# Kernel optimization log

Hardware: AMD Instinct MI355X
Metric: run time of the kernel (lower is better)

The kernel has to match this reference:

```python
import jax, jax.numpy as jnp
import numpy as np

EMBED_DIM = 1024
ATTN_DIM = 128
B, S = 4, 2048


def setup_inputs() -> dict:
    key = jax.random.key(0)
    k1, k2, k3, k4 = jax.random.split(key, 4)
    embedded = jax.random.normal(k1, (B, S, EMBED_DIM), dtype=jnp.float32)
    # torch nn.Linear weights are [out_features, in_features]
    scale = 1.0 / np.sqrt(EMBED_DIM)
    Wk = jax.random.uniform(k2, (ATTN_DIM, EMBED_DIM), dtype=jnp.float32, minval=-scale, maxval=scale)
    Wq = jax.random.uniform(k3, (ATTN_DIM, EMBED_DIM), dtype=jnp.float32, minval=-scale, maxval=scale)
    Wv = jax.random.uniform(k4, (ATTN_DIM, EMBED_DIM), dtype=jnp.float32, minval=-scale, maxval=scale)
    return {"embedded": embedded, "Wk": Wk, "Wq": Wq, "Wv": Wv}


def reference(embedded, Wk, Wq, Wv):
    # projections (no bias): x @ W.T
    k = jnp.einsum('bse,ae->bsa', embedded, Wk)  # [B,S,A]
    q = jnp.einsum('bse,ae->bsa', embedded, Wq)
    v = jnp.einsum('bse,ae->bsa', embedded, Wv)
    ad = k.shape[-1]
    scores = jnp.einsum('bqa,bka->bqk', q, k) / jnp.sqrt(jnp.float32(ad))  # [B,S,S]
    causal = jnp.tril(jnp.ones((scores.shape[1], scores.shape[1]), dtype=bool))
    scores = jnp.where(causal, scores, -jnp.inf)
    probs = jax.nn.softmax(scores, axis=-1)
    out = jnp.einsum('bqk,bka->bqa', probs, v)
    return jnp.round(out, 4)
```

## Files before the change

kernel.cpp:

```cpp
#include <hip/hip_runtime.h>
#include <hip/hip_bf16.h>
#include <math.h>

#define B 4
#define S 2048
#define E 1024
#define A 128
#define CHUNK 256
#define NCHMAX 8

typedef __attribute__((ext_vector_type(8))) short short8;
typedef __attribute__((ext_vector_type(4))) float floatx4;

static __device__ __forceinline__ short f2bf(float f) {
  union { float f; unsigned u; } c;
  c.f = f;
  unsigned r = (c.u + 0x7fffu + ((c.u >> 16) & 1u)) >> 16;
  return (short)r;
}
static __device__ __forceinline__ unsigned f2bf2(float x, float y) {
  __hip_bfloat162 h = __float22bfloat162_rn(float2{x, y});
  union { __hip_bfloat162 h; unsigned u; } c;
  c.h = h;
  return c.u;
}

__global__ __launch_bounds__(256) void wconv(
    const float* __restrict__ Wq,
    const float* __restrict__ Wk,
    const float* __restrict__ Wv,
    short* __restrict__ Wbf) {
  const int which = blockIdx.y;
  const float* Wp = (which == 0) ? Wq : (which == 1) ? Wk : Wv;
  short* o = Wbf + (size_t)which * A * E;
  const int f = blockIdx.x * 256 + threadIdx.x;
  const float4 v = *(const float4*)&Wp[(size_t)f * 4];
  uint2 p; p.x = f2bf2(v.x, v.y); p.y = f2bf2(v.z, v.w);
  *(uint2*)&o[(size_t)f * 4] = p;
}

__global__ __launch_bounds__(256) void proj_gemm(
    const float* __restrict__ X,
    const short* __restrict__ Wbf,
    short* __restrict__ Qbf,
    short* __restrict__ Kbf,
    short* __restrict__ Vt) {
  __shared__ short As[64 * 64];
  __shared__ short Bs[128 * 64];

  const int m0 = blockIdx.x * 64;
  const int which = blockIdx.y;
  const short* Wpb = Wbf + (size_t)which * A * E;

  const int tid = threadIdx.x;
  const int wave = tid >> 6;
  const int lane = tid & 63;
  const int mh = wave & 1;
  const int nh = wave >> 1;
  const int l16 = lane & 15;
  const int quad = lane >> 4;

  int xbase[4], wbase[4], aoff[4], boff[4];
#pragma unroll
  for (int i = 0; i < 4; ++i) {
    const int fa = tid + i * 256;
    const int arow = fa >> 4, ac4 = fa & 15;
    xbase[i] = (m0 + arow) * E + ac4 * 4;
    aoff[i] = arow * 64 + (((ac4 >> 1) ^ (arow & 7)) << 3) + ((ac4 & 1) << 2);
    const int fb = tid + i * 256;
    const int brow = fb >> 3, bc8 = fb & 7;
    wbase[i] = brow * E + bc8 * 8;
    boff[i] = brow * 64 + ((bc8 ^ (brow & 7)) << 3);
  }

  int arb[2], brb[4], swz[2];
#pragma unroll
  for (int ms = 0; ms < 2; ++ms) arb[ms] = (mh * 32 + ms * 16 + l16) * 64;
#pragma unroll
  for (int nt = 0; nt < 4; ++nt) brb[nt] = (nh * 64 + nt * 16 + l16) * 64;
#pragma unroll
  for (int ks = 0; ks < 2; ++ks) swz[ks] = (((ks * 4 + quad) ^ (l16 & 7)) << 3);

  floatx4 acc[2][4] = {};
  float4 apl0[4], apl1[4];
  short8 bpl0[4], bpl1[4];

#pragma unroll
  for (int i = 0; i < 4; ++i) {
    apl0[i] = *(const float4*)&X[xbase[i]];
    bpl0[i] = *(const short8*)&Wpb[wbase[i]];
    apl1[i] = *(const float4*)&X[xbase[i] + 64];
    bpl1[i] = *(const short8*)&Wpb[wbase[i] + 64];
  }

#define PROJ_BODY(APL, BPL, KNEXT)                                            \
  do {                                                                        \
    __syncthreads();                                                          \
    _Pragma("unroll") for (int i = 0; i < 4; ++i) {                           \
      uint2 pk; pk.x = f2bf2(APL[i].x, APL[i].y);                             \
      pk.y = f2bf2(APL[i].z, APL[i].w);                                       \
      *(uint2*)&As[aoff[i]] = pk;                                             \
      *(short8*)&Bs[boff[i]] = BPL[i];                                        \
    }                                                                         \
    __syncthreads();                                                          \
    if ((KNEXT) < E) {                                                        \
      _Pragma("unroll") for (int i = 0; i < 4; ++i) {                         \
        APL[i] = *(const float4*)&X[xbase[i] + (KNEXT)];                      \
        BPL[i] = *(const short8*)&Wpb[wbase[i] + (KNEXT)];                    \
      }                                                                       \
    }                                                                         \
    short8 afr[2][2], bfr[4][2];                                              \
    _Pragma("unroll") for (int ms = 0; ms < 2; ++ms)                          \
      _Pragma("unroll") for (int ks = 0; ks < 2; ++ks)                        \
        afr[ms][ks] = *(const short8*)&As[arb[ms] + swz[ks]];                 \
    _Pragma("unroll") for (int nt = 0; nt < 4; ++nt)                          \
      _Pragma("unroll") for (int ks = 0; ks < 2; ++ks)                        \
        bfr[nt][ks] = *(const short8*)&Bs[brb[nt] + swz[ks]];                 \
    _Pragma("unroll") for (int ms = 0; ms < 2; ++ms)                          \
      _Pragma("unroll") for (int nt = 0; nt < 4; ++nt)                        \
        _Pragma("unroll") for (int ks = 0; ks < 2; ++ks)                      \
          acc[ms][nt] = __builtin_amdgcn_mfma_f32_16x16x32_bf16(              \
              afr[ms][ks], bfr[nt][ks], acc[ms][nt], 0, 0, 0);                \
  } while (0)

  for (int k0 = 0; k0 < E; k0 += 128) {
    PROJ_BODY(apl0, bpl0, k0 + 128);
    PROJ_BODY(apl1, bpl1, k0 + 192);
  }
#undef PROJ_BODY

  const float qscale = 0.08838834764831845f;
#pragma unroll
  for (int ms = 0; ms < 2; ++ms) {
#pragma unroll
    for (int nt = 0; nt < 4; ++nt) {
      const int n = nh * 64 + nt * 16 + l16;
      const int mbase = m0 + mh * 32 + ms * 16 + quad * 4;
      if (which == 2) {
        const int b = mbase >> 11, s = mbase & (S - 1);
        short4 p;
        p.x = f2bf(acc[ms][nt][0]); p.y = f2bf(acc[ms][nt][1]);
        p.z = f2bf(acc[ms][nt][2]); p.w = f2bf(acc[ms][nt][3]);
        *(short4*)&Vt[((size_t)b * A + n) * S + s] = p;
      } else {
        short* Outp = (which == 0) ? Qbf : Kbf;
        const float sc = (which == 0) ? qscale : 1.0f;
#pragma unroll
        for (int r = 0; r < 4; ++r)
          Outp[(size_t)(mbase + r) * A + n] = f2bf(acc[ms][nt][r] * sc);
      }
    }
  }
}

#define LP 68
__global__ __launch_bounds__(256) void attn_part(
    const short* __restrict__ Qbf,
    const short* __restrict__ Kbf,
    const short* __restrict__ Vt,
    float* __restrict__ Opart,
    float* __restrict__ Lpart) {
  __shared__ short Ks[64 * 128];
  __shared__ short Vs[128 * 64];
  __shared__ short Ps[4][16 * LP];

  const int rev = (int)gridDim.x - 1 - (int)blockIdx.x;
  const int qt = rev >> 3;
  const int chunk = rev & 7;
  const int b = qt >> 5;
  const int q0 = (qt & 31) << 6;
  const int nk = q0 + 64;
  const int kstart = chunk * CHUNK;
  if (kstart >= nk) return;
  const int kend = min(kstart + CHUNK, nk);

  const int tid = threadIdx.x;
  const int wave = tid >> 6;
  const int lane = tid & 63;
  const int l16 = lane & 15;
  const int quad = lane >> 4;

  int kgb[4], vgb[4], kwoff[4], vwoff[4];
#pragma unroll
  for (int i = 0; i < 4; ++i) {
    const int f = tid + i * 256;
    const int krow = f >> 4, kc8 = f & 15;
    kgb[i] = krow * A + kc8 * 8;
    kwoff[i] = krow * 128 + ((kc8 ^ (krow & 7)) << 3);
    const int vrow = f >> 3, vc8 = f & 7;
    vgb[i] = vrow * S + vc8 * 8;
    vwoff[i] = vrow * 64 + ((vc8 ^ (vrow & 7)) << 3);
  }

  int swz[4];
#pragma unroll
  for (int ks = 0; ks < 4; ++ks) swz[ks] = (((ks * 4 + quad) ^ (l16 & 7)) << 3);

  short8 qfr[4];
  {
    const size_t qrow = (size_t)(b * S + q0 + wave * 16 + l16);
#pragma unroll
    for (int ks = 0; ks < 4; ++ks)
      qfr[ks] = *(const short8*)&Qbf[qrow * A + ks * 32 + quad * 8];
  }

  float l_acc[4] = {0.f, 0.f, 0.f, 0.f};
  floatx4 oacc[8] = {};

  const int myrow = q0 + wave * 16 + quad * 4;
  const short* Kbase = Kbf + (size_t)b * S * A;
  const short* Vbase = Vt + (size_t)b * A * S;

  short8 kplf[4], vplf[4];
#pragma unroll
  for (int i = 0; i < 4; ++i) {
    kplf[i] = *(const short8*)&Kbase[kstart * A + kgb[i]];
    vplf[i] = *(const short8*)&Vbase[vgb[i] + kstart];
  }

  for (int j0 = kstart; j0 < kend; j0 += 64) {
    __syncthreads();
#pragma unroll
    for (int i = 0; i < 4; ++i) {
      *(short8*)&Ks[kwoff[i]] = kplf[i];
      *(short8*)&Vs[vwoff[i]] = vplf[i];
    }
    __syncthreads();

    if (j0 + 64 < kend) {
#pragma unroll
      for (int i = 0; i < 4; ++i) {
        kplf[i] = *(const short8*)&Kbase[(j0 + 64) * A + kgb[i]];
        vplf[i] = *(const short8*)&Vbase[vgb[i] + j0 + 64];
      }
    }

    floatx4 sc[4];
#pragma unroll
    for (int nt = 0; nt < 4; ++nt) {
      floatx4 c = {};
#pragma unroll
      for (int ks = 0; ks < 4; ++ks) {
        const short8 bfr = *(const short8*)&Ks[(nt * 16 + l16) * 128 + swz[ks]];
        c = __builtin_amdgcn_mfma_f32_16x16x32_bf16(qfr[ks], bfr, c, 0, 0, 0);
      }
      sc[nt] = c;
    }

#pragma unroll
    for (int nt = 0; nt < 4; ++nt) {
      const int key = j0 + nt * 16 + l16;
#pragma unroll
      for (int r = 0; r < 4; ++r) {
        const float p = (key > myrow + r) ? 0.f : __expf(sc[nt][r]);
        sc[nt][r] = p;
        l_acc[r] += p;
      }
    }

#pragma unroll
    for (int nt = 0; nt < 4; ++nt)
#pragma unroll
      for (int r = 0; r < 4; ++r)
        Ps[wave][(quad * 4 + r) * LP + nt * 16 + l16] = f2bf(sc[nt][r]);

    short8 pfr[2];
#pragma unroll
    for (int ks = 0; ks < 2; ++ks)
      pfr[ks] = *(const short8*)&Ps[wave][l16 * LP + ks * 32 + quad * 8];

#pragma unroll
    for (int nt = 0; nt < 8; ++nt) {
#pragma unroll
      for (int ks = 0; ks < 2; ++ks) {
        const short8 vfr = *(const short8*)&Vs[(nt * 16 + l16) * 64 + swz[ks]];
        oacc[nt] = __builtin_amdgcn_mfma_f32_16x16x32_bf16(pfr[ks], vfr, oacc[nt], 0, 0, 0);
      }
    }
  }

  const int slot = qt * NCHMAX + chunk;
  float* op = Opart + (size_t)slot * 64 * 128;
  const int lr = wave * 16 + quad * 4;
#pragma unroll
  for (int nt = 0; nt < 8; ++nt)
#pragma unroll
    for (int r = 0; r < 4; ++r)
      op[(lr + r) * 128 + nt * 16 + l16] = oacc[nt][r];

#pragma unroll
  for (int r = 0; r < 4; ++r) {
    float l = l_acc[r];
    l += __shfl_xor(l, 1);
    l += __shfl_xor(l, 2);
    l += __shfl_xor(l, 4);
    l += __shfl_xor(l, 8);
    if (l16 == 0) Lpart[slot * 64 + lr + r] = l;
  }
}

__global__ __launch_bounds__(256) void attn_reduce(
    const float* __restrict__ Opart,
    const float* __restrict__ Lpart,
    float* __restrict__ Out) {
  const int qt = blockIdx.x >> 1;
  const int half = blockIdx.x & 1;
  const int b = qt >> 5;
  const int q0 = (qt & 31) << 6;
  const int nch = (q0 + 64 + CHUNK - 1) / CHUNK;

  const int tid = threadIdx.x;
  const int lr = half * 32 + (tid >> 3);
  const int c0 = (tid & 7) * 16;

  float ltot = 0.f;
  for (int c = 0; c < nch; ++c) ltot += Lpart[(qt * NCHMAX + c) * 64 + lr];
  const float inv = 1.f / ltot;

  float4 acc[4] = {};
  for (int c = 0; c < nch; ++c) {
    const float4* op = (const float4*)
        (Opart + ((size_t)(qt * NCHMAX + c) * 64 + lr) * 128 + c0);
#pragma unroll
    for (int i = 0; i < 4; ++i) {
      const float4 v = op[i];
      acc[i].x += v.x; acc[i].y += v.y; acc[i].z += v.z; acc[i].w += v.w;
    }
  }

  float4* o = (float4*)(Out + (size_t)(b * S + q0 + lr) * A + c0);
#pragma unroll
  for (int i = 0; i < 4; ++i) {
    float4 v = acc[i];
    v.x *= inv; v.y *= inv; v.z *= inv; v.w *= inv;
    o[i] = v;
  }
}

extern "C" void kernel_launch(void* const* d_in, const int* in_sizes, int n_in,
                              void* d_out, int out_size, void* d_ws, size_t ws_size,
                              hipStream_t stream) {
  const float* X  = (const float*)d_in[0];
  const float* Wk = (const float*)d_in[1];
  const float* Wq = (const float*)d_in[2];
  const float* Wv = (const float*)d_in[3];
  float* Out = (float*)d_out;

  const size_t qkv_elems = (size_t)B * S * A;
  short* Qbf = (short*)d_ws;
  short* Kbf = Qbf + qkv_elems;
  short* Vt  = Kbf + qkv_elems;
  float* Opart = (float*)(Vt + qkv_elems);
  float* Lpart = Opart + (size_t)1024 * 64 * 128;
  short* Wbf = (short*)(Lpart + (size_t)1024 * 64);

  wconv<<<dim3(A * E / 4 / 256, 3), 256, 0, stream>>>(Wq, Wk, Wv, Wbf);
  dim3 pgrid(B * S / 64, 3);
  proj_gemm<<<pgrid, 256, 0, stream>>>(X, Wbf, Qbf, Kbf, Vt);
  attn_part<<<(B * S / 64) * NCHMAX, 256, 0, stream>>>(Qbf, Kbf, Vt, Opart, Lpart);
  attn_reduce<<<B * S / 64 * 2, 256, 0, stream>>>(Opart, Lpart, Out);
}
```

Baseline: 120.5 us.

## Fuse split-K attention reduction into partial kernel via atomic last-block combine

Removes the separate attn_reduce launch. The last chunk block to finish for each query tile, detected with an atomic counter that proj_gemm resets, sums the partial outputs and normalizes them. Tiles covered by a single chunk write the normalized output directly and skip the partial buffers. The key chunk size doubles to 512, which halves the number of partials but gives each block more serial work and less parallelism.

```diff
diff --git a/kernel.cpp b/kernel.cpp
--- a/kernel.cpp
+++ b/kernel.cpp
@@ -6,8 +6,8 @@
 #define S 2048
 #define E 1024
 #define A 128
-#define CHUNK 256
-#define NCHMAX 8
+#define CHUNK 512
+#define NCHMAX 4
 
 typedef __attribute__((ext_vector_type(8))) short short8;
 typedef __attribute__((ext_vector_type(4))) float floatx4;
@@ -44,9 +44,12 @@
     const short* __restrict__ Wbf,
     short* __restrict__ Qbf,
     short* __restrict__ Kbf,
-    short* __restrict__ Vt) {
+    short* __restrict__ Vt,
+    int* __restrict__ cnt) {
   __shared__ short As[64 * 64];
   __shared__ short Bs[128 * 64];
+
+  if (blockIdx.y == 0 && threadIdx.x == 0) cnt[blockIdx.x] = 0;
 
   const int m0 = blockIdx.x * 64;
   const int which = blockIdx.y;
@@ -159,20 +162,24 @@
     const short* __restrict__ Kbf,
     const short* __restrict__ Vt,
     float* __restrict__ Opart,
-    float* __restrict__ Lpart) {
+    float* __restrict__ Lpart,
+    int* __restrict__ cnt,
+    float* __restrict__ Out) {
   __shared__ short Ks[64 * 128];
   __shared__ short Vs[128 * 64];
   __shared__ short Ps[4][16 * LP];
+  __shared__ int s_last;
 
   const int rev = (int)gridDim.x - 1 - (int)blockIdx.x;
-  const int qt = rev >> 3;
-  const int chunk = rev & 7;
+  const int qt = rev >> 2;
+  const int chunk = rev & 3;
   const int b = qt >> 5;
   const int q0 = (qt & 31) << 6;
   const int nk = q0 + 64;
   const int kstart = chunk * CHUNK;
   if (kstart >= nk) return;
   const int kend = min(kstart + CHUNK, nk);
+  const int nch = (nk + CHUNK - 1) / CHUNK;
 
   const int tid = threadIdx.x;
   const int wave = tid >> 6;
@@ -279,15 +286,8 @@
     }
   }
 
-  const int slot = qt * NCHMAX + chunk;
-  float* op = Opart + (size_t)slot * 64 * 128;
   const int lr = wave * 16 + quad * 4;
-#pragma unroll
-  for (int nt = 0; nt < 8; ++nt)
-#pragma unroll
-    for (int r = 0; r < 4; ++r)
-      op[(lr + r) * 128 + nt * 16 + l16] = oacc[nt][r];
-
+  float lsum[4];
 #pragma unroll
   for (int r = 0; r < 4; ++r) {
     float l = l_acc[r];
@@ -295,43 +295,65 @@
     l += __shfl_xor(l, 2);
     l += __shfl_xor(l, 4);
     l += __shfl_xor(l, 8);
-    if (l16 == 0) Lpart[slot * 64 + lr + r] = l;
-  }
-}
-
-__global__ __launch_bounds__(256) void attn_reduce(
-    const float* __restrict__ Opart,
-    const float* __restrict__ Lpart,
-    float* __restrict__ Out) {
-  const int qt = blockIdx.x >> 1;
-  const int half = blockIdx.x & 1;
-  const int b = qt >> 5;
-  const int q0 = (qt & 31) << 6;
-  const int nch = (q0 + 64 + CHUNK - 1) / CHUNK;
-
-  const int tid = threadIdx.x;
-  const int lr = half * 32 + (tid >> 3);
-  const int c0 = (tid & 7) * 16;
+    lsum[r] = l;
+  }
+
+  if (nch == 1) {
+    float inv4[4];
+#pragma unroll
+    for (int r = 0; r < 4; ++r) inv4[r] = 1.f / lsum[r];
+    float* o = Out + (size_t)(b * S + q0 + lr) * A;
+#pragma unroll
+    for (int nt = 0; nt < 8; ++nt)
+#pragma unroll
+      for (int r = 0; r < 4; ++r)
+        o[(size_t)r * A + nt * 16 + l16] = oacc[nt][r] * inv4[r];
+    return;
+  }
+
+  const int slot = qt * NCHMAX + chunk;
+  float* op = Opart + (size_t)slot * 64 * 128;
+#pragma unroll
+  for (int nt = 0; nt < 8; ++nt)
+#pragma unroll
+    for (int r = 0; r < 4; ++r)
+      op[(lr + r) * 128 + nt * 16 + l16] = oacc[nt][r];
+  if (l16 == 0) {
+#pragma unroll
+    for (int r = 0; r < 4; ++r) Lpart[slot * 64 + lr + r] = lsum[r];
+  }
+
+  __syncthreads();
+  if (tid == 0) {
+    const int old = __hip_atomic_fetch_add(&cnt[qt], 1, __ATOMIC_ACQ_REL,
+                                           __HIP_MEMORY_SCOPE_AGENT);
+    s_last = (old == nch - 1) ? 1 : 0;
+  }
+  __syncthreads();
+  if (!s_last) return;
+
+  const int lr2 = tid >> 2;
+  const int c0 = (tid & 3) * 32;
 
   float ltot = 0.f;
-  for (int c = 0; c < nch; ++c) ltot += Lpart[(qt * NCHMAX + c) * 64 + lr];
+  for (int c = 0; c < nch; ++c) ltot += Lpart[(qt * NCHMAX + c) * 64 + lr2];
   const float inv = 1.f / ltot;
 
-  float4 acc[4] = {};
+  float4 acc2[8] = {};
   for (int c = 0; c < nch; ++c) {
-    const float4* op = (const float4*)
-        (Opart + ((size_t)(qt * NCHMAX + c) * 64 + lr) * 128 + c0);
-#pragma unroll
-    for (int i = 0; i < 4; ++i) {
-      const float4 v = op[i];
-      acc[i].x += v.x; acc[i].y += v.y; acc[i].z += v.z; acc[i].w += v.w;
-    }
-  }
-
-  float4* o = (float4*)(Out + (size_t)(b * S + q0 + lr) * A + c0);
-#pragma unroll
-  for (int i = 0; i < 4; ++i) {
-    float4 v = acc[i];
+    const float4* op2 = (const float4*)
+        (Opart + ((size_t)(qt * NCHMAX + c) * 64 + lr2) * 128 + c0);
+#pragma unroll
+    for (int i = 0; i < 8; ++i) {
+      const float4 v = op2[i];
+      acc2[i].x += v.x; acc2[i].y += v.y; acc2[i].z += v.z; acc2[i].w += v.w;
+    }
+  }
+
+  float4* o = (float4*)(Out + (size_t)(b * S + q0 + lr2) * A + c0);
+#pragma unroll
+  for (int i = 0; i < 8; ++i) {
+    float4 v = acc2[i];
     v.x *= inv; v.y *= inv; v.z *= inv; v.w *= inv;
     o[i] = v;
   }
@@ -351,12 +373,12 @@
   short* Kbf = Qbf + qkv_elems;
   short* Vt  = Kbf + qkv_elems;
   float* Opart = (float*)(Vt + qkv_elems);
-  float* Lpart = Opart + (size_t)1024 * 64 * 128;
-  short* Wbf = (short*)(Lpart + (size_t)1024 * 64);
+  float* Lpart = Opart + (size_t)512 * 64 * 128;
+  short* Wbf = (short*)(Lpart + (size_t)512 * 64);
+  int* cnt = (int*)(Wbf + (size_t)3 * A * E);
 
   wconv<<<dim3(A * E / 4 / 256, 3), 256, 0, stream>>>(Wq, Wk, Wv, Wbf);
   dim3 pgrid(B * S / 64, 3);
-  proj_gemm<<<pgrid, 256, 0, stream>>>(X, Wbf, Qbf, Kbf, Vt);
-  attn_part<<<(B * S / 64) * NCHMAX, 256, 0, stream>>>(Qbf, Kbf, Vt, Opart, Lpart);
-  attn_reduce<<<B * S / 64 * 2, 256, 0, stream>>>(Opart, Lpart, Out);
-}
+  proj_gemm<<<pgrid, 256, 0, stream>>>(X, Wbf, Qbf, Kbf, Vt, cnt);
+  attn_part<<<(B * S / 64) * NCHMAX, 256, 0, stream>>>(Qbf, Kbf, Vt, Opart, Lpart, cnt, Out);
+}
```

Result: slower. 132.1 us (+9.6%).
